# Kernel tuning notes

Hardware: AMD Instinct MI355X
Metric: run time of the kernel (lower is better)

The kernel has to match this reference:

```python
import jax, jax.numpy as jnp
import numpy as np

B, N, D_POINTS, D_MODEL = 2, 2048, 32, 512


def _gather(feat, idx):
    # feat: [B, N, C], idx: [B, N, K] -> [B, N, K, C]
    return jax.vmap(lambda f, i: f[i])(feat, idx)


def setup_inputs() -> dict:
    key = jax.random.key(0)
    ks = jax.random.split(key, 20)
    def lin(k, fan_in, fan_out):
        bound = 1.0 / np.sqrt(fan_in)
        return jax.random.uniform(k, (fan_in, fan_out), jnp.float32, -bound, bound)
    def bias(k, fan_in, fan_out):
        bound = 1.0 / np.sqrt(fan_in)
        return jax.random.uniform(k, (fan_out,), jnp.float32, -bound, bound)
    return {
        "xyz": jax.random.normal(ks[0], (B, N, 3), jnp.float32),
        "points": jax.random.normal(ks[1], (B, N, D_POINTS), jnp.float32),
        "fc1_w": lin(ks[2], D_POINTS, D_MODEL), "fc1_b": bias(ks[3], D_POINTS, D_MODEL),
        "fc2_w": lin(ks[4], D_MODEL, D_POINTS), "fc2_b": bias(ks[5], D_MODEL, D_POINTS),
        "delta_w1": lin(ks[6], 3, D_MODEL), "delta_b1": bias(ks[7], 3, D_MODEL),
        "delta_w2": lin(ks[8], D_MODEL, D_MODEL), "delta_b2": bias(ks[9], D_MODEL, D_MODEL),
        "gamma_w1": lin(ks[10], D_MODEL, D_MODEL), "gamma_b1": bias(ks[11], D_MODEL, D_MODEL),
        "gamma_w2": lin(ks[12], D_MODEL, D_MODEL), "gamma_b2": bias(ks[13], D_MODEL, D_MODEL),
        "wq": lin(ks[14], D_MODEL, D_MODEL),
        "wk": lin(ks[15], D_MODEL, D_MODEL),
        "wv": lin(ks[16], D_MODEL, D_MODEL),
        "knn_k": 16,
    }


def reference(xyz, points, fc1_w, fc1_b, fc2_w, fc2_b,
              delta_w1, delta_b1, delta_w2, delta_b2,
              gamma_w1, gamma_b1, gamma_w2, gamma_b2,
              wq, wk, wv, knn_k):
    # square_distance: [B, N, N]
    sq = jnp.sum(xyz * xyz, axis=-1)
    dists = sq[:, :, None] + sq[:, None, :] - 2.0 * jnp.einsum('bnc,bmc->bnm', xyz, xyz)
    # knn: k smallest distances (argsort[:, :, :k] equivalent)
    _, knn_idx = jax.lax.top_k(-dists, knn_k)           # [B, N, K]
    knn_xyz = _gather(xyz, knn_idx)                      # [B, N, K, 3]

    pre = points
    x = points @ fc1_w + fc1_b                           # [B, N, d_model]
    q = x @ wq                                           # [B, N, d_model]
    k = _gather(x @ wk, knn_idx)                         # [B, N, K, d_model]
    v = _gather(x @ wv, knn_idx)                         # [B, N, K, d_model]

    # positional encoding MLP on delta xyz
    delta = xyz[:, :, None, :] - knn_xyz                 # [B, N, K, 3]
    pos_enc = jax.nn.relu(delta @ delta_w1 + delta_b1) @ delta_w2 + delta_b2

    # gamma MLP on (q - k + pos_enc)
    a = q[:, :, None, :] - k + pos_enc
    a = jax.nn.relu(a @ gamma_w1 + gamma_b1) @ gamma_w2 + gamma_b2

    scale = jnp.asarray(np.sqrt(D_MODEL), a.dtype)
    attn = jax.nn.softmax(a / scale, axis=-2)            # softmax over neighbors, per channel

    res = jnp.sum(attn * (v + pos_enc), axis=2)          # einsum 'bmnf,bmnf->bmf'
    res = res @ fc2_w + fc2_b + pre                      # [B, N, d_points]
    return res, attn
```

## Files before the change

kernel.cpp:

```cpp
#include <hip/hip_runtime.h>
#include <hip/hip_bf16.h>
#include <math.h>

typedef __bf16 bf16_t;
typedef float f32x4 __attribute__((ext_vector_type(4)));
typedef bf16_t bf16x8 __attribute__((ext_vector_type(8)));

#define BM 128
#define BN 128
#define BKT 32
#define NT 16

#define GLD_LDS16(gp, lp) __builtin_amdgcn_global_load_lds( \
    (const __attribute__((address_space(1))) void*)(gp), \
    (__attribute__((address_space(3))) void*)(lp), 16, 0, 0)

struct TC7 { const float* src[7]; bf16_t* dst[7]; };
__global__ __launch_bounds__(256) void tcast7_kernel(TC7 tc) {
  int job = blockIdx.x >> 10;
  int idx = (blockIdx.x & 1023) * 256 + threadIdx.x;
  if (job < 4) {
    int n = idx >> 9, k = idx & 511;
    tc.dst[job][idx] = (bf16_t)tc.src[job][k * 512 + n];
  } else {
    tc.dst[job][idx] = (bf16_t)tc.src[job][idx];
  }
}

__global__ __launch_bounds__(256) void cc_kernel(const float* __restrict__ db2, const float* __restrict__ gw1,
                                                 const float* __restrict__ gb1, float* __restrict__ cc) {
  int n = blockIdx.x * 256 + threadIdx.x;
  float s = gb1[n];
  for (int d = 0; d < 512; ++d) s = fmaf(db2[d], gw1[d * 512 + n], s);
  cc[n] = s;
}

__global__ __launch_bounds__(256) void knn_kernel(const float* __restrict__ xyz, int* __restrict__ knn) {
  __shared__ float sx[2048], sy[2048], sz[2048], sq[2048];
  int tid = threadIdx.x;
  int lane = tid & 63, wave = tid >> 6;
  int gq = blockIdx.x * 4 + wave;
  int b  = gq >> 11;
  int base = b << 11;
  for (int p = tid; p < 2048; p += 256) {
    float x = xyz[(base + p) * 3 + 0];
    float y = xyz[(base + p) * 3 + 1];
    float z = xyz[(base + p) * 3 + 2];
    sx[p] = x; sy[p] = y; sz[p] = z;
    sq[p] = __fadd_rn(__fadd_rn(__fmul_rn(x, x), __fmul_rn(y, y)), __fmul_rn(z, z));
  }
  __syncthreads();
  int iq = gq & 2047;
  float qx = sx[iq], qy = sy[iq], qz = sz[iq], sqi = sq[iq];

  unsigned long long key[32];
  #pragma unroll
  for (int j = 0; j < 32; ++j) {
    int p = lane + j * 64;
    float d = __fmul_rn(sx[p], qx);
    d = fmaf(sy[p], qy, d);
    d = fmaf(sz[p], qz, d);
    float dist = __fsub_rn(__fadd_rn(sqi, sq[p]), __fmul_rn(2.0f, d));
    unsigned int bits = __float_as_uint(dist);
    unsigned int sk = bits ^ (unsigned int)(((int)bits >> 31) | 0x80000000);
    key[j] = ((unsigned long long)sk << 32) | (unsigned int)p;
  }

  int r = 0;
  #pragma unroll 1
  for (int s = 0; s < 16; ++s) {
    unsigned long long m = key[0];
    #pragma unroll
    for (int j = 1; j < 32; ++j) m = (key[j] < m) ? key[j] : m;
    #pragma unroll
    for (int off = 32; off > 0; off >>= 1) {
      unsigned long long o = (unsigned long long)__shfl_xor((long long)m, off);
      if (o < m) m = o;
    }
    if (lane == s) r = base + (int)(m & 0xFFFFFFFFu);
    #pragma unroll
    for (int j = 0; j < 32; ++j) key[j] = (key[j] == m) ? ~0ULL : key[j];
  }
  if (lane < 16) knn[gq * 16 + lane] = r;
}

__global__ __launch_bounds__(256) void xfeat_kernel(const float* __restrict__ points, const float* __restrict__ fc1_w,
                                                    const float* __restrict__ fc1_b, bf16_t* __restrict__ xb) {
  __shared__ float p[32];
  int m = blockIdx.x, tid = threadIdx.x;
  if (tid < 32) p[tid] = points[m * 32 + tid];
  __syncthreads();
  for (int c = tid; c < 512; c += 256) {
    float a = fc1_b[c];
    #pragma unroll
    for (int kk = 0; kk < 32; ++kk) a = fmaf(p[kk], fc1_w[kk * 512 + c], a);
    xb[m * 512 + c] = (bf16_t)a;
  }
}

__global__ __launch_bounds__(256) void final_kernel(const float* __restrict__ res_mid, const float* __restrict__ fc2_w,
                                                    const float* __restrict__ fc2_b, const float* __restrict__ points,
                                                    float* __restrict__ out) {
  int oid = blockIdx.x * 256 + threadIdx.x;
  int m = oid >> 5, c = oid & 31;
  float a = fc2_b[c];
  const float* rm = res_mid + m * 512;
  for (int kk = 0; kk < 512; ++kk) a = fmaf(rm[kk], fc2_w[kk * 32 + c], a);
  out[oid] = a + points[oid];
}

struct GP {
  const bf16_t* A; const bf16_t* Bt;
  bf16_t* Cb; const float* bias; int ldc;
  const float* xyz; const int* knn; const float* dw1; const float* db1;
  const float* cc; const bf16_t* qkg;
  const bf16_t* vb; const bf16_t* peb; float* attn; float* res_mid;
  const bf16_t* Aj[3]; bf16_t* Cbj[3];
};

template <int SRC, int EPI>
__global__ __launch_bounds__(256) void gemm_kernel(GP gp) {
  __shared__ bf16_t Alds[2 * BM * BKT];
  __shared__ bf16_t Blds[2 * BN * BKT];
  __shared__ float  wl[(SRC == 2) ? 4 * 512 : 8];
  int tid  = threadIdx.x;
  int lane = tid & 63, wave = tid >> 6;
  int wr = wave >> 1, wc = wave & 1;
  int lr = lane & 15, lg = lane >> 4;

  int gx = gridDim.x;
  int nwg = gx * gridDim.y;
  int orig = blockIdx.y * gx + blockIdx.x;
  int cpx = nwg >> 3;
  int swz = (orig & 7) * cpx + (orig >> 3);
  int bx = swz % gx;
  int by = swz / gx;
  int n0 = bx * BN;
  int m0 = ((EPI == 4) ? (by & 3) : by) * BM;
  const bf16_t* Aptr = (EPI == 4) ? gp.Aj[by >> 2] : gp.A;

  f32x4 acc[4][4];
  #pragma unroll
  for (int i = 0; i < 4; ++i)
    #pragma unroll
    for (int j = 0; j < 4; ++j) acc[i][j] = (f32x4){0.f, 0.f, 0.f, 0.f};

  int rS2 = tid >> 2;
  int sl  = tid & 3;
  int swb = (rS2 >> 1) & 3;
  int scS = ((sl ^ swb) << 3);

  float dx0, dy0, dz0, dx1, dy1, dz1;
  if (SRC == 2) {
    for (int c = tid; c < 512; c += 256) {
      wl[c]        = gp.dw1[c];
      wl[512 + c]  = gp.dw1[512 + c];
      wl[1024 + c] = gp.dw1[1024 + c];
      wl[1536 + c] = gp.db1[c];
    }
    int m_a = m0 + rS2, m_b = m0 + rS2 + 64;
    int ga = m_a >> 4, ja = gp.knn[m_a];
    int gb = m_b >> 4, jb = gp.knn[m_b];
    dx0 = gp.xyz[ga * 3 + 0] - gp.xyz[ja * 3 + 0];
    dy0 = gp.xyz[ga * 3 + 1] - gp.xyz[ja * 3 + 1];
    dz0 = gp.xyz[ga * 3 + 2] - gp.xyz[ja * 3 + 2];
    dx1 = gp.xyz[gb * 3 + 0] - gp.xyz[jb * 3 + 0];
    dy1 = gp.xyz[gb * 3 + 1] - gp.xyz[jb * 3 + 1];
    dz1 = gp.xyz[gb * 3 + 2] - gp.xyz[jb * 3 + 2];
    __syncthreads();
  }

  auto stageA = [&](int t, int buf) {
    int k0 = t * BKT;
    if (SRC == 0) {
      GLD_LDS16(Aptr + (size_t)(m0 + rS2) * 512 + k0 + scS,       Alds + buf * (BM * BKT) + tid * 8);
      GLD_LDS16(Aptr + (size_t)(m0 + 64 + rS2) * 512 + k0 + scS,  Alds + buf * (BM * BKT) + 2048 + tid * 8);
    } else {
      int cb = k0 + sl * 8;
      f32x4 w0a = *(const f32x4*)(&wl[cb]),        w0b = *(const f32x4*)(&wl[cb + 4]);
      f32x4 w1a = *(const f32x4*)(&wl[512 + cb]),  w1b = *(const f32x4*)(&wl[512 + cb + 4]);
      f32x4 w2a = *(const f32x4*)(&wl[1024 + cb]), w2b = *(const f32x4*)(&wl[1024 + cb + 4]);
      f32x4 bba = *(const f32x4*)(&wl[1536 + cb]), bbb = *(const f32x4*)(&wl[1536 + cb + 4]);
      bf16_t* Ab = Alds + buf * (BM * BKT);
      bf16x8 o;
      #pragma unroll
      for (int u = 0; u < 4; ++u) {
        float h = fmaf(dz0, w2a[u], fmaf(dy0, w1a[u], dx0 * w0a[u])) + bba[u];
        o[u] = (bf16_t)fmaxf(h, 0.0f);
      }
      #pragma unroll
      for (int u = 0; u < 4; ++u) {
        float h = fmaf(dz0, w2b[u], fmaf(dy0, w1b[u], dx0 * w0b[u])) + bbb[u];
        o[4 + u] = (bf16_t)fmaxf(h, 0.0f);
      }
      *(bf16x8*)(&Ab[rS2 * BKT + (scS ^ 0)]) = o;
      #pragma unroll
      for (int u = 0; u < 4; ++u) {
        float h = fmaf(dz1, w2a[u], fmaf(dy1, w1a[u], dx1 * w0a[u])) + bba[u];
        o[u] = (bf16_t)fmaxf(h, 0.0f);
      }
      #pragma unroll
      for (int u = 0; u < 4; ++u) {
        float h = fmaf(dz1, w2b[u], fmaf(dy1, w1b[u], dx1 * w0b[u])) + bbb[u];
        o[4 + u] = (bf16_t)fmaxf(h, 0.0f);
      }
      *(bf16x8*)(&Ab[(rS2 + 64) * BKT + (scS ^ 0)]) = o;
    }
  };
  auto stageB = [&](int t, int buf) {
    int k0 = t * BKT;
    GLD_LDS16(gp.Bt + (size_t)(n0 + rS2) * 512 + k0 + scS,       Blds + buf * (BN * BKT) + tid * 8);
    GLD_LDS16(gp.Bt + (size_t)(n0 + 64 + rS2) * 512 + k0 + scS,  Blds + buf * (BN * BKT) + 2048 + tid * 8);
  };
  auto mfmaPhase = [&](int cur) {
    const bf16_t* Ab = Alds + cur * (BM * BKT);
    const bf16_t* Bb = Blds + cur * (BN * BKT);
    bf16x8 af[4], bfr[4];
    #pragma unroll
    for (int mi = 0; mi < 4; ++mi) {
      int rr = wr * 64 + mi * 16 + lr;
      af[mi] = *(const bf16x8*)(&Ab[rr * BKT + ((lg ^ ((rr >> 1) & 3)) << 3)]);
    }
    #pragma unroll
    for (int nj = 0; nj < 4; ++nj) {
      int rr = wc * 64 + nj * 16 + lr;
      bfr[nj] = *(const bf16x8*)(&Bb[rr * BKT + ((lg ^ ((rr >> 1) & 3)) << 3)]);
    }
    #pragma unroll
    for (int mi = 0; mi < 4; ++mi)
      #pragma unroll
      for (int nj = 0; nj < 4; ++nj)
        acc[mi][nj] = __builtin_amdgcn_mfma_f32_16x16x32_bf16(af[mi], bfr[nj], acc[mi][nj], 0, 0, 0);
  };

  stageA(0, 0);
  stageB(0, 0);

  #pragma unroll 1
  for (int t = 0; t < NT; ++t) {
    int cur = t & 1;
    if (t + 1 < NT) {
      stageA(t + 1, cur ^ 1);
      stageB(t + 1, cur ^ 1);
      if (SRC == 0) asm volatile("s_waitcnt vmcnt(4)" ::: "memory");
      else          asm volatile("s_waitcnt vmcnt(2) lgkmcnt(0)" ::: "memory");
    } else {
      asm volatile("s_waitcnt vmcnt(0) lgkmcnt(0)" ::: "memory");
    }
    __builtin_amdgcn_s_barrier();
    mfmaPhase(cur);
    __builtin_amdgcn_s_barrier();
  }

  if (EPI == 4) {
    bf16_t* CbT = gp.Cbj[by >> 2];
    #pragma unroll
    for (int mi = 0; mi < 4; ++mi)
      #pragma unroll
      for (int nj = 0; nj < 4; ++nj) {
        int col = n0 + wc * 64 + nj * 16 + lr;
        #pragma unroll
        for (int r = 0; r < 4; ++r) {
          int row = m0 + wr * 64 + mi * 16 + lg * 4 + r;
          CbT[(size_t)col * 512 + row] = (bf16_t)acc[mi][nj][r];
        }
      }
  } else if (EPI == 6) {
    #pragma unroll
    for (int mi = 0; mi < 4; ++mi)
      #pragma unroll
      for (int nj = 0; nj < 4; ++nj) {
        int col = n0 + wc * 64 + nj * 16 + lr;
        int part = col >> 9, c = col & 511;
        #pragma unroll
        for (int r = 0; r < 4; ++r) {
          int row = m0 + wr * 64 + mi * 16 + lg * 4 + r;
          gp.Cb[((size_t)part * 4096 + row) * 512 + c] = (bf16_t)acc[mi][nj][r];
        }
      }
  } else if (EPI == 1) {
    #pragma unroll
    for (int mi = 0; mi < 4; ++mi)
      #pragma unroll
      for (int nj = 0; nj < 4; ++nj) {
        int col = n0 + wc * 64 + nj * 16 + lr;
        float bv = gp.bias[col];
        #pragma unroll
        for (int r = 0; r < 4; ++r) {
          int row = m0 + wr * 64 + mi * 16 + lg * 4 + r;
          gp.Cb[(size_t)row * 512 + col] = (bf16_t)(acc[mi][nj][r] + bv);
        }
      }
  } else if (EPI == 2) {
    #pragma unroll
    for (int mi = 0; mi < 4; ++mi) {
      int g = (m0 + wr * 64 + mi * 16) >> 4;
      #pragma unroll
      for (int nj = 0; nj < 4; ++nj) {
        int col = n0 + wc * 64 + nj * 16 + lr;
        float ccv = gp.cc[col];
        float qgv = (float)gp.qkg[((size_t)4096 + g) * 512 + col];
        #pragma unroll
        for (int r = 0; r < 4; ++r) {
          int row = m0 + wr * 64 + mi * 16 + lg * 4 + r;
          int j = gp.knn[row];
          float kgv = (float)gp.qkg[((size_t)2 * 4096 + j) * 512 + col];
          float hv = acc[mi][nj][r] + ccv + qgv - kgv;
          gp.Cb[(size_t)row * 512 + col] = (bf16_t)fmaxf(hv, 0.0f);
        }
      }
    }
  } else {
    const float scale = 22.62741699796952f;
    #pragma unroll
    for (int mi = 0; mi < 4; ++mi) {
      int g = (m0 + wr * 64 + mi * 16) >> 4;
      #pragma unroll
      for (int nj = 0; nj < 4; ++nj) {
        int col = n0 + wc * 64 + nj * 16 + lr;
        float sv[4];
        float mx = -INFINITY;
        #pragma unroll
        for (int r = 0; r < 4; ++r) {
          sv[r] = (acc[mi][nj][r] + gp.bias[col]) / scale;
          mx = fmaxf(mx, sv[r]);
        }
        mx = fmaxf(mx, __shfl_xor(mx, 16));
        mx = fmaxf(mx, __shfl_xor(mx, 32));
        float e[4], sum = 0.f;
        #pragma unroll
        for (int r = 0; r < 4; ++r) { e[r] = expf(sv[r] - mx); sum += e[r]; }
        sum += __shfl_xor(sum, 16);
        sum += __shfl_xor(sum, 32);
        float part = 0.f;
        #pragma unroll
        for (int r = 0; r < 4; ++r) {
          int row = g * 16 + lg * 4 + r;
          float at = e[r] / sum;
          int j = gp.knn[row];
          float vv  = (float)gp.vb[(size_t)j * 512 + col];
          float pev = (float)gp.peb[(size_t)row * 512 + col];
          part = fmaf(at, vv + pev, part);
          gp.attn[(size_t)row * 512 + col] = at;
        }
        part += __shfl_xor(part, 16);
        part += __shfl_xor(part, 32);
        if (lg == 0) gp.res_mid[(size_t)g * 512 + col] = part;
      }
    }
  }
}

extern "C" void kernel_launch(void* const* d_in, const int* in_sizes, int n_in,
                              void* d_out, int out_size, void* d_ws, size_t ws_size,
                              hipStream_t stream) {
  const float* xyz    = (const float*)d_in[0];
  const float* points = (const float*)d_in[1];
  const float* fc1_w  = (const float*)d_in[2];
  const float* fc1_b  = (const float*)d_in[3];
  const float* fc2_w  = (const float*)d_in[4];
  const float* fc2_b  = (const float*)d_in[5];
  const float* dw1    = (const float*)d_in[6];
  const float* db1    = (const float*)d_in[7];
  const float* dw2    = (const float*)d_in[8];
  const float* db2    = (const float*)d_in[9];
  const float* gw1    = (const float*)d_in[10];
  const float* gb1    = (const float*)d_in[11];
  const float* gw2    = (const float*)d_in[12];
  const float* gb2    = (const float*)d_in[13];
  const float* wq     = (const float*)d_in[14];
  const float* wk     = (const float*)d_in[15];
  const float* wv     = (const float*)d_in[16];

  float* out = (float*)d_out;
  float* attn = out + 131072;

  char* w = (char*)d_ws;
  bf16_t* wBig   = (bf16_t*)w; w += (size_t)1536 * 512 * 2;
  bf16_t* dw2T   = (bf16_t*)w; w += (size_t)512 * 512 * 2;
  bf16_t* gw1T   = (bf16_t*)w; w += (size_t)512 * 512 * 2;
  bf16_t* gw2T   = (bf16_t*)w; w += (size_t)512 * 512 * 2;
  bf16_t* dw2b   = (bf16_t*)w; w += (size_t)512 * 512 * 2;
  bf16_t* wqb    = (bf16_t*)w; w += (size_t)512 * 512 * 2;
  bf16_t* wkb    = (bf16_t*)w; w += (size_t)512 * 512 * 2;
  bf16_t* WpT    = (bf16_t*)w; w += (size_t)512 * 512 * 2;
  float*  cc     = (float*)w;  w += (size_t)512 * 4;
  int*    knn    = (int*)w;    w += (size_t)65536 * 4;
  bf16_t* xb     = (bf16_t*)w; w += (size_t)4096 * 512 * 2;
  bf16_t* vqkg   = (bf16_t*)w; w += (size_t)3 * 4096 * 512 * 2;
  bf16_t* peb    = (bf16_t*)w; w += (size_t)65536 * 512 * 2;
  bf16_t* h2     = (bf16_t*)w; w += (size_t)65536 * 512 * 2;
  float*  res_mid= (float*)w;  w += (size_t)4096 * 512 * 4;

  TC7 tc;
  tc.src[0] = wv;  tc.dst[0] = wBig;
  tc.src[1] = dw2; tc.dst[1] = dw2T;
  tc.src[2] = gw1; tc.dst[2] = gw1T;
  tc.src[3] = gw2; tc.dst[3] = gw2T;
  tc.src[4] = dw2; tc.dst[4] = dw2b;
  tc.src[5] = wq;  tc.dst[5] = wqb;
  tc.src[6] = wk;  tc.dst[6] = wkb;
  tcast7_kernel<<<7168, 256, 0, stream>>>(tc);

  knn_kernel<<<1024, 256, 0, stream>>>(xyz, knn);
  xfeat_kernel<<<4096, 256, 0, stream>>>(points, fc1_w, fc1_b, xb);
  cc_kernel<<<2, 256, 0, stream>>>(db2, gw1, gb1, cc);

  GP gwp{};
  gwp.Bt = gw1T;
  gwp.Aj[0] = dw2b; gwp.Cbj[0] = WpT;
  gwp.Aj[1] = wqb;  gwp.Cbj[1] = wBig + (size_t)512 * 512;
  gwp.Aj[2] = wkb;  gwp.Cbj[2] = wBig + (size_t)2 * 512 * 512;
  gemm_kernel<0, 4><<<dim3(4, 12), 256, 0, stream>>>(gwp);

  GP gq{};
  gq.A = xb; gq.Bt = wBig; gq.Cb = vqkg; gq.ldc = 1536;
  gemm_kernel<0, 6><<<dim3(12, 32), 256, 0, stream>>>(gq);

  GP gpe{};
  gpe.Bt = dw2T; gpe.Cb = peb; gpe.bias = db2;
  gpe.xyz = xyz; gpe.knn = knn; gpe.dw1 = dw1; gpe.db1 = db1;
  gemm_kernel<2, 1><<<dim3(4, 512), 256, 0, stream>>>(gpe);

  GP gg{};
  gg.Bt = WpT; gg.Cb = h2;
  gg.xyz = xyz; gg.knn = knn; gg.dw1 = dw1; gg.db1 = db1;
  gg.cc = cc; gg.qkg = vqkg;
  gemm_kernel<2, 2><<<dim3(4, 512), 256, 0, stream>>>(gg);

  GP gs{};
  gs.A = h2; gs.Bt = gw2T; gs.bias = gb2;
  gs.knn = knn; gs.vb = vqkg; gs.peb = peb; gs.attn = attn; gs.res_mid = res_mid;
  gemm_kernel<0, 3><<<dim3(4, 512), 256, 0, stream>>>(gs);

  final_kernel<<<512, 256, 0, stream>>>(res_mid, fc2_w, fc2_b, points, out);
}
```

Measured before the change: 436.7 us.

## Fuse pos-enc, gamma-hidden and softmax GEMMs into one register-resident kernel

Replaces the three per-neighbor GEMM launches (pos-enc, gamma layer 1, gamma layer 2 with softmax epilogue) with a single fused kernel. Each 64-row block keeps h2 and pos_enc in packed bf16 registers and re-shuffles them through a small LDS bounce buffer as MFMA A-operands. This removes the 64 MB peb and h2 intermediates and their global round trips. In exchange it carries heavy register pressure (64 u32 arrays), recomputes the h1 fragments twice, and uses a narrower N=64 M tile that may lower MFMA efficiency and occupancy.

```diff
diff --git a/kernel.cpp b/kernel.cpp
--- a/kernel.cpp
+++ b/kernel.cpp
@@ -5,15 +5,24 @@
 typedef __bf16 bf16_t;
 typedef float f32x4 __attribute__((ext_vector_type(4)));
 typedef bf16_t bf16x8 __attribute__((ext_vector_type(8)));
-
-#define BM 128
-#define BN 128
-#define BKT 32
-#define NT 16
+typedef unsigned int u32;
+typedef u32 u32x2 __attribute__((ext_vector_type(2)));
+typedef u32 u32x4 __attribute__((ext_vector_type(4)));
+typedef unsigned short u16x4 __attribute__((ext_vector_type(4)));
 
 #define GLD_LDS16(gp, lp) __builtin_amdgcn_global_load_lds( \
     (const __attribute__((address_space(1))) void*)(gp), \
     (__attribute__((address_space(3))) void*)(lp), 16, 0, 0)
+
+static __device__ __forceinline__ unsigned short f2b(float f) {
+  union { bf16_t b; unsigned short s; } u; u.b = (bf16_t)f; return u.s;
+}
+static __device__ __forceinline__ float b2f(unsigned short s) {
+  union { unsigned int i; float f; } u; u.i = ((unsigned)s) << 16; return u.f;
+}
+static __device__ __forceinline__ u32 packbf(float a, float b) {
+  return (u32)f2b(a) | ((u32)f2b(b) << 16);
+}
 
 struct TC7 { const float* src[7]; bf16_t* dst[7]; };
 __global__ __launch_bounds__(256) void tcast7_kernel(TC7 tc) {
@@ -110,19 +119,14 @@
 }
 
 struct GP {
-  const bf16_t* A; const bf16_t* Bt;
-  bf16_t* Cb; const float* bias; int ldc;
-  const float* xyz; const int* knn; const float* dw1; const float* db1;
-  const float* cc; const bf16_t* qkg;
-  const bf16_t* vb; const bf16_t* peb; float* attn; float* res_mid;
+  const bf16_t* A; const bf16_t* Bt; bf16_t* Cb; int ldc;
   const bf16_t* Aj[3]; bf16_t* Cbj[3];
 };
 
-template <int SRC, int EPI>
+template <int EPI>
 __global__ __launch_bounds__(256) void gemm_kernel(GP gp) {
-  __shared__ bf16_t Alds[2 * BM * BKT];
-  __shared__ bf16_t Blds[2 * BN * BKT];
-  __shared__ float  wl[(SRC == 2) ? 4 * 512 : 8];
+  __shared__ bf16_t Alds[2 * 128 * 32];
+  __shared__ bf16_t Blds[2 * 128 * 32];
   int tid  = threadIdx.x;
   int lane = tid & 63, wave = tid >> 6;
   int wr = wave >> 1, wc = wave & 1;
@@ -135,8 +139,8 @@
   int swz = (orig & 7) * cpx + (orig >> 3);
   int bx = swz % gx;
   int by = swz / gx;
-  int n0 = bx * BN;
-  int m0 = ((EPI == 4) ? (by & 3) : by) * BM;
+  int n0 = bx * 128;
+  int m0 = ((EPI == 4) ? (by & 3) : by) * 128;
   const bf16_t* Aptr = (EPI == 4) ? gp.Aj[by >> 2] : gp.A;
 
   f32x4 acc[4][4];
@@ -146,109 +150,52 @@
     for (int j = 0; j < 4; ++j) acc[i][j] = (f32x4){0.f, 0.f, 0.f, 0.f};
 
   int rS2 = tid >> 2;
-  int sl  = tid & 3;
   int swb = (rS2 >> 1) & 3;
-  int scS = ((sl ^ swb) << 3);
-
-  float dx0, dy0, dz0, dx1, dy1, dz1;
-  if (SRC == 2) {
-    for (int c = tid; c < 512; c += 256) {
-      wl[c]        = gp.dw1[c];
-      wl[512 + c]  = gp.dw1[512 + c];
-      wl[1024 + c] = gp.dw1[1024 + c];
-      wl[1536 + c] = gp.db1[c];
-    }
-    int m_a = m0 + rS2, m_b = m0 + rS2 + 64;
-    int ga = m_a >> 4, ja = gp.knn[m_a];
-    int gb = m_b >> 4, jb = gp.knn[m_b];
-    dx0 = gp.xyz[ga * 3 + 0] - gp.xyz[ja * 3 + 0];
-    dy0 = gp.xyz[ga * 3 + 1] - gp.xyz[ja * 3 + 1];
-    dz0 = gp.xyz[ga * 3 + 2] - gp.xyz[ja * 3 + 2];
-    dx1 = gp.xyz[gb * 3 + 0] - gp.xyz[jb * 3 + 0];
-    dy1 = gp.xyz[gb * 3 + 1] - gp.xyz[jb * 3 + 1];
-    dz1 = gp.xyz[gb * 3 + 2] - gp.xyz[jb * 3 + 2];
-    __syncthreads();
-  }
+  int scS = (((tid & 3) ^ swb) << 3);
 
   auto stageA = [&](int t, int buf) {
-    int k0 = t * BKT;
-    if (SRC == 0) {
-      GLD_LDS16(Aptr + (size_t)(m0 + rS2) * 512 + k0 + scS,       Alds + buf * (BM * BKT) + tid * 8);
-      GLD_LDS16(Aptr + (size_t)(m0 + 64 + rS2) * 512 + k0 + scS,  Alds + buf * (BM * BKT) + 2048 + tid * 8);
-    } else {
-      int cb = k0 + sl * 8;
-      f32x4 w0a = *(const f32x4*)(&wl[cb]),        w0b = *(const f32x4*)(&wl[cb + 4]);
-      f32x4 w1a = *(const f32x4*)(&wl[512 + cb]),  w1b = *(const f32x4*)(&wl[512 + cb + 4]);
-      f32x4 w2a = *(const f32x4*)(&wl[1024 + cb]), w2b = *(const f32x4*)(&wl[1024 + cb + 4]);
-      f32x4 bba = *(const f32x4*)(&wl[1536 + cb]), bbb = *(const f32x4*)(&wl[1536 + cb + 4]);
-      bf16_t* Ab = Alds + buf * (BM * BKT);
-      bf16x8 o;
-      #pragma unroll
-      for (int u = 0; u < 4; ++u) {
-        float h = fmaf(dz0, w2a[u], fmaf(dy0, w1a[u], dx0 * w0a[u])) + bba[u];
-        o[u] = (bf16_t)fmaxf(h, 0.0f);
-      }
-      #pragma unroll
-      for (int u = 0; u < 4; ++u) {
-        float h = fmaf(dz0, w2b[u], fmaf(dy0, w1b[u], dx0 * w0b[u])) + bbb[u];
-        o[4 + u] = (bf16_t)fmaxf(h, 0.0f);
-      }
-      *(bf16x8*)(&Ab[rS2 * BKT + (scS ^ 0)]) = o;
-      #pragma unroll
-      for (int u = 0; u < 4; ++u) {
-        float h = fmaf(dz1, w2a[u], fmaf(dy1, w1a[u], dx1 * w0a[u])) + bba[u];
-        o[u] = (bf16_t)fmaxf(h, 0.0f);
-      }
-      #pragma unroll
-      for (int u = 0; u < 4; ++u) {
-        float h = fmaf(dz1, w2b[u], fmaf(dy1, w1b[u], dx1 * w0b[u])) + bbb[u];
-        o[4 + u] = (bf16_t)fmaxf(h, 0.0f);
-      }
-      *(bf16x8*)(&Ab[(rS2 + 64) * BKT + (scS ^ 0)]) = o;
-    }
+    int k0 = t * 32;
+    GLD_LDS16(Aptr + (size_t)(m0 + rS2) * 512 + k0 + scS,       Alds + buf * 4096 + tid * 8);
+    GLD_LDS16(Aptr + (size_t)(m0 + 64 + rS2) * 512 + k0 + scS,  Alds + buf * 4096 + 2048 + tid * 8);
   };
   auto stageB = [&](int t, int buf) {
-    int k0 = t * BKT;
-    GLD_LDS16(gp.Bt + (size_t)(n0 + rS2) * 512 + k0 + scS,       Blds + buf * (BN * BKT) + tid * 8);
-    GLD_LDS16(gp.Bt + (size_t)(n0 + 64 + rS2) * 512 + k0 + scS,  Blds + buf * (BN * BKT) + 2048 + tid * 8);
+    int k0 = t * 32;
+    GLD_LDS16(gp.Bt + (size_t)(n0 + rS2) * 512 + k0 + scS,       Blds + buf * 4096 + tid * 8);
+    GLD_LDS16(gp.Bt + (size_t)(n0 + 64 + rS2) * 512 + k0 + scS,  Blds + buf * 4096 + 2048 + tid * 8);
   };
-  auto mfmaPhase = [&](int cur) {
-    const bf16_t* Ab = Alds + cur * (BM * BKT);
-    const bf16_t* Bb = Blds + cur * (BN * BKT);
+
+  stageA(0, 0);
+  stageB(0, 0);
+
+  #pragma unroll 1
+  for (int t = 0; t < 16; ++t) {
+    int cur = t & 1;
+    if (t + 1 < 16) {
+      stageA(t + 1, cur ^ 1);
+      stageB(t + 1, cur ^ 1);
+      asm volatile("s_waitcnt vmcnt(4)" ::: "memory");
+    } else {
+      asm volatile("s_waitcnt vmcnt(0)" ::: "memory");
+    }
+    __builtin_amdgcn_s_barrier();
+    const bf16_t* Ab = Alds + cur * 4096;
+    const bf16_t* Bb = Blds + cur * 4096;
     bf16x8 af[4], bfr[4];
     #pragma unroll
     for (int mi = 0; mi < 4; ++mi) {
       int rr = wr * 64 + mi * 16 + lr;
-      af[mi] = *(const bf16x8*)(&Ab[rr * BKT + ((lg ^ ((rr >> 1) & 3)) << 3)]);
+      af[mi] = *(const bf16x8*)(&Ab[rr * 32 + ((lg ^ ((rr >> 1) & 3)) << 3)]);
     }
     #pragma unroll
     for (int nj = 0; nj < 4; ++nj) {
       int rr = wc * 64 + nj * 16 + lr;
-      bfr[nj] = *(const bf16x8*)(&Bb[rr * BKT + ((lg ^ ((rr >> 1) & 3)) << 3)]);
+      bfr[nj] = *(const bf16x8*)(&Bb[rr * 32 + ((lg ^ ((rr >> 1) & 3)) << 3)]);
     }
     #pragma unroll
     for (int mi = 0; mi < 4; ++mi)
       #pragma unroll
       for (int nj = 0; nj < 4; ++nj)
         acc[mi][nj] = __builtin_amdgcn_mfma_f32_16x16x32_bf16(af[mi], bfr[nj], acc[mi][nj], 0, 0, 0);
-  };
-
-  stageA(0, 0);
-  stageB(0, 0);
-
-  #pragma unroll 1
-  for (int t = 0; t < NT; ++t) {
-    int cur = t & 1;
-    if (t + 1 < NT) {
-      stageA(t + 1, cur ^ 1);
-      stageB(t + 1, cur ^ 1);
-      if (SRC == 0) asm volatile("s_waitcnt vmcnt(4)" ::: "memory");
-      else          asm volatile("s_waitcnt vmcnt(2) lgkmcnt(0)" ::: "memory");
-    } else {
-      asm volatile("s_waitcnt vmcnt(0) lgkmcnt(0)" ::: "memory");
-    }
-    __builtin_amdgcn_s_barrier();
-    mfmaPhase(cur);
     __builtin_amdgcn_s_barrier();
   }
 
@@ -265,7 +212,7 @@
           CbT[(size_t)col * 512 + row] = (bf16_t)acc[mi][nj][r];
         }
       }
-  } else if (EPI == 6) {
+  } else {
     #pragma unroll
     for (int mi = 0; mi < 4; ++mi)
       #pragma unroll
@@ -278,75 +225,214 @@
           gp.Cb[((size_t)part * 4096 + row) * 512 + c] = (bf16_t)acc[mi][nj][r];
         }
       }
-  } else if (EPI == 1) {
-    #pragma unroll
-    for (int mi = 0; mi < 4; ++mi)
-      #pragma unroll
-      for (int nj = 0; nj < 4; ++nj) {
-        int col = n0 + wc * 64 + nj * 16 + lr;
-        float bv = gp.bias[col];
-        #pragma unroll
-        for (int r = 0; r < 4; ++r) {
-          int row = m0 + wr * 64 + mi * 16 + lg * 4 + r;
-          gp.Cb[(size_t)row * 512 + col] = (bf16_t)(acc[mi][nj][r] + bv);
-        }
+  }
+}
+
+struct FP {
+  const float* xyz; const int* knn;
+  const float* dw1; const float* db1; const float* db2; const float* cc; const float* gb2;
+  const bf16_t* WpT; const bf16_t* dw2T; const bf16_t* gw2T;
+  const bf16_t* vqkg;
+  float* attn; float* res_mid;
+};
+
+__global__ __launch_bounds__(256, 2) void fused_kernel(FP fp) {
+  __shared__ float  wl[3584];
+  __shared__ bf16_t Bst[2 * 128 * 32];
+  __shared__ u32    bounce[4 * 256];
+
+  int tid = threadIdx.x, lane = tid & 63, w = tid >> 6;
+  int lr = lane & 15, lg = lane >> 4;
+
+  int nwg = gridDim.x, orig = blockIdx.x, cpx = nwg >> 3;
+  int bid = (orig & 7) * cpx + (orig >> 3);
+  int m0 = bid * 64;
+  int g  = (m0 >> 4) + w;
+  int myrow = m0 + w * 16 + lr;
+  int j_lane = fp.knn[myrow];
+  float dx = fp.xyz[g * 3 + 0] - fp.xyz[j_lane * 3 + 0];
+  float dy = fp.xyz[g * 3 + 1] - fp.xyz[j_lane * 3 + 1];
+  float dz = fp.xyz[g * 3 + 2] - fp.xyz[j_lane * 3 + 2];
+
+  for (int c = tid; c < 1536; c += 256) wl[c] = fp.dw1[c];
+  for (int c = tid; c < 512; c += 256) {
+    wl[1536 + c] = fp.db1[c];
+    wl[2048 + c] = fp.cc[c];
+    wl[2560 + c] = fp.db2[c];
+    wl[3072 + c] = fp.gb2[c];
+  }
+  __syncthreads();
+
+  auto h1frag = [&](int st) -> bf16x8 {
+    int c = st * 32 + lg * 8;
+    f32x4 w0a = *(const f32x4*)&wl[c],        w0b = *(const f32x4*)&wl[c + 4];
+    f32x4 w1a = *(const f32x4*)&wl[512 + c],  w1b = *(const f32x4*)&wl[512 + c + 4];
+    f32x4 w2a = *(const f32x4*)&wl[1024 + c], w2b = *(const f32x4*)&wl[1024 + c + 4];
+    f32x4 ba  = *(const f32x4*)&wl[1536 + c], bb = *(const f32x4*)&wl[1536 + c + 4];
+    bf16x8 o;
+    #pragma unroll
+    for (int u = 0; u < 4; ++u) {
+      float h = fmaf(dz, w2a[u], fmaf(dy, w1a[u], dx * w0a[u])) + ba[u];
+      o[u] = (bf16_t)fmaxf(h, 0.0f);
+    }
+    #pragma unroll
+    for (int u = 0; u < 4; ++u) {
+      float h = fmaf(dz, w2b[u], fmaf(dy, w1b[u], dx * w0b[u])) + bb[u];
+      o[4 + u] = (bf16_t)fmaxf(h, 0.0f);
+    }
+    return o;
+  };
+
+  int rS2 = tid >> 2;
+  int scS = (((tid & 3) ^ ((rS2 >> 1) & 3)) << 3);
+  auto stage = [&](const bf16_t* Bt, int base, int st, int buf) {
+    GLD_LDS16(Bt + (size_t)(base + rS2) * 512 + st * 32 + scS,      Bst + buf * 4096 + tid * 8);
+    GLD_LDS16(Bt + (size_t)(base + 64 + rS2) * 512 + st * 32 + scS, Bst + buf * 4096 + 2048 + tid * 8);
+  };
+  auto bfrag = [&](int buf, int tt) -> bf16x8 {
+    int rr = tt * 16 + lr;
+    return *(const bf16x8*)(&Bst[buf * 4096 + rr * 32 + ((lg ^ ((rr >> 1) & 3)) << 3)]);
+  };
+
+  u32 h2pk[32][2];
+  u32 pepk[32][2];
+
+  #pragma unroll
+  for (int mc = 0; mc < 4; ++mc) {
+    f32x4 acc1[8];
+    #pragma unroll
+    for (int i = 0; i < 8; ++i) acc1[i] = (f32x4){0.f, 0.f, 0.f, 0.f};
+    stage(fp.WpT, mc * 128, 0, 0);
+    #pragma unroll 1
+    for (int st = 0; st < 16; ++st) {
+      if (st < 15) {
+        stage(fp.WpT, mc * 128, st + 1, (st & 1) ^ 1);
+        asm volatile("s_waitcnt vmcnt(2)" ::: "memory");
+      } else {
+        asm volatile("s_waitcnt vmcnt(0)" ::: "memory");
       }
-  } else if (EPI == 2) {
-    #pragma unroll
-    for (int mi = 0; mi < 4; ++mi) {
-      int g = (m0 + wr * 64 + mi * 16) >> 4;
-      #pragma unroll
-      for (int nj = 0; nj < 4; ++nj) {
-        int col = n0 + wc * 64 + nj * 16 + lr;
-        float ccv = gp.cc[col];
-        float qgv = (float)gp.qkg[((size_t)4096 + g) * 512 + col];
-        #pragma unroll
-        for (int r = 0; r < 4; ++r) {
-          int row = m0 + wr * 64 + mi * 16 + lg * 4 + r;
-          int j = gp.knn[row];
-          float kgv = (float)gp.qkg[((size_t)2 * 4096 + j) * 512 + col];
-          float hv = acc[mi][nj][r] + ccv + qgv - kgv;
-          gp.Cb[(size_t)row * 512 + col] = (bf16_t)fmaxf(hv, 0.0f);
-        }
+      __builtin_amdgcn_s_barrier();
+      bf16x8 bh = h1frag(st);
+      #pragma unroll
+      for (int tt = 0; tt < 8; ++tt)
+        acc1[tt] = __builtin_amdgcn_mfma_f32_16x16x32_bf16(bfrag(st & 1, tt), bh, acc1[tt], 0, 0, 0);
+      __builtin_amdgcn_s_barrier();
+    }
+    #pragma unroll
+    for (int tt = 0; tt < 8; ++tt) {
+      int c0 = mc * 128 + tt * 16 + lg * 4;
+      u16x4 kg4 = *(const u16x4*)((const unsigned short*)fp.vqkg + ((size_t)2 * 4096 + j_lane) * 512 + c0);
+      u16x4 qg4 = *(const u16x4*)((const unsigned short*)fp.vqkg + ((size_t)4096 + g) * 512 + c0);
+      f32x4 cc4 = *(const f32x4*)&wl[2048 + c0];
+      float hv[4];
+      #pragma unroll
+      for (int r = 0; r < 4; ++r)
+        hv[r] = fmaxf(acc1[tt][r] + cc4[r] + b2f(qg4[r]) - b2f(kg4[r]), 0.0f);
+      h2pk[mc * 8 + tt][0] = packbf(hv[0], hv[1]);
+      h2pk[mc * 8 + tt][1] = packbf(hv[2], hv[3]);
+    }
+  }
+
+  #pragma unroll
+  for (int nc = 0; nc < 4; ++nc) {
+    f32x4 acc2[8];
+    #pragma unroll
+    for (int i = 0; i < 8; ++i) acc2[i] = (f32x4){0.f, 0.f, 0.f, 0.f};
+    stage(fp.dw2T, nc * 128, 0, 0);
+    #pragma unroll 1
+    for (int st = 0; st < 16; ++st) {
+      if (st < 15) {
+        stage(fp.dw2T, nc * 128, st + 1, (st & 1) ^ 1);
+        asm volatile("s_waitcnt vmcnt(2)" ::: "memory");
+      } else {
+        asm volatile("s_waitcnt vmcnt(0)" ::: "memory");
       }
-    }
-  } else {
-    const float scale = 22.62741699796952f;
-    #pragma unroll
-    for (int mi = 0; mi < 4; ++mi) {
-      int g = (m0 + wr * 64 + mi * 16) >> 4;
-      #pragma unroll
-      for (int nj = 0; nj < 4; ++nj) {
-        int col = n0 + wc * 64 + nj * 16 + lr;
-        float sv[4];
-        float mx = -INFINITY;
-        #pragma unroll
-        for (int r = 0; r < 4; ++r) {
-          sv[r] = (acc[mi][nj][r] + gp.bias[col]) / scale;
-          mx = fmaxf(mx, sv[r]);
-        }
-        mx = fmaxf(mx, __shfl_xor(mx, 16));
-        mx = fmaxf(mx, __shfl_xor(mx, 32));
-        float e[4], sum = 0.f;
-        #pragma unroll
-        for (int r = 0; r < 4; ++r) { e[r] = expf(sv[r] - mx); sum += e[r]; }
-        sum += __shfl_xor(sum, 16);
-        sum += __shfl_xor(sum, 32);
-        float part = 0.f;
-        #pragma unroll
-        for (int r = 0; r < 4; ++r) {
-          int row = g * 16 + lg * 4 + r;
-          float at = e[r] / sum;
-          int j = gp.knn[row];
-          float vv  = (float)gp.vb[(size_t)j * 512 + col];
-          float pev = (float)gp.peb[(size_t)row * 512 + col];
-          part = fmaf(at, vv + pev, part);
-          gp.attn[(size_t)row * 512 + col] = at;
-        }
-        part += __shfl_xor(part, 16);
-        part += __shfl_xor(part, 32);
-        if (lg == 0) gp.res_mid[(size_t)g * 512 + col] = part;
+      __builtin_amdgcn_s_barrier();
+      bf16x8 ah = h1frag(st);
+      #pragma unroll
+      for (int tt = 0; tt < 8; ++tt)
+        acc2[tt] = __builtin_amdgcn_mfma_f32_16x16x32_bf16(ah, bfrag(st & 1, tt), acc2[tt], 0, 0, 0);
+      __builtin_amdgcn_s_barrier();
+    }
+    #pragma unroll
+    for (int tt = 0; tt < 8; ++tt) {
+      int col = nc * 128 + tt * 16 + lr;
+      float d2 = wl[2560 + col];
+      pepk[nc * 8 + tt][0] = packbf(acc2[tt][0] + d2, acc2[tt][1] + d2);
+      pepk[nc * 8 + tt][1] = packbf(acc2[tt][2] + d2, acc2[tt][3] + d2);
+    }
+  }
+
+  u32* bw = &bounce[w * 256];
+  int wrOff = lane * 4;
+  int rdA = (lr + ((lg & 1) << 5)) * 4 + (lg >> 1) * 2;
+  int rdB = rdA + 64;
+  int jr[4];
+  #pragma unroll
+  for (int r = 0; r < 4; ++r) jr[r] = __shfl(j_lane, lg * 4 + r);
+
+  const float scale = 22.62741699796952f;
+
+  #pragma unroll
+  for (int nc = 0; nc < 4; ++nc) {
+    f32x4 acc3[8];
+    #pragma unroll
+    for (int i = 0; i < 8; ++i) acc3[i] = (f32x4){0.f, 0.f, 0.f, 0.f};
+    stage(fp.gw2T, nc * 128, 0, 0);
+
+#define P3STEP(ST) { \
+    if ((ST) < 15) { stage(fp.gw2T, nc * 128, (ST) + 1, ((ST) & 1) ^ 1); \
+                     asm volatile("s_waitcnt vmcnt(2)" ::: "memory"); } \
+    else           { asm volatile("s_waitcnt vmcnt(0)" ::: "memory"); } \
+    __builtin_amdgcn_s_barrier(); \
+    *(u32x4*)(bw + wrOff) = (u32x4){h2pk[2*(ST)][0], h2pk[2*(ST)][1], h2pk[2*(ST)+1][0], h2pk[2*(ST)+1][1]}; \
+    asm volatile("s_waitcnt lgkmcnt(0)" ::: "memory"); \
+    union { bf16x8 v; u32x2 h[2]; } afu; \
+    afu.h[0] = *(const u32x2*)(bw + rdA); \
+    afu.h[1] = *(const u32x2*)(bw + rdB); \
+    _Pragma("unroll") \
+    for (int tt = 0; tt < 8; ++tt) \
+      acc3[tt] = __builtin_amdgcn_mfma_f32_16x16x32_bf16(afu.v, bfrag((ST) & 1, tt), acc3[tt], 0, 0, 0); \
+    __builtin_amdgcn_s_barrier(); }
+
+    P3STEP(0)  P3STEP(1)  P3STEP(2)  P3STEP(3)
+    P3STEP(4)  P3STEP(5)  P3STEP(6)  P3STEP(7)
+    P3STEP(8)  P3STEP(9)  P3STEP(10) P3STEP(11)
+    P3STEP(12) P3STEP(13) P3STEP(14) P3STEP(15)
+#undef P3STEP
+
+    #pragma unroll
+    for (int tt = 0; tt < 8; ++tt) {
+      int col = nc * 128 + tt * 16 + lr;
+      float gb2v = wl[3072 + col];
+      float sv[4];
+      float mx = -INFINITY;
+      #pragma unroll
+      for (int r = 0; r < 4; ++r) {
+        sv[r] = (acc3[tt][r] + gb2v) / scale;
+        mx = fmaxf(mx, sv[r]);
       }
+      mx = fmaxf(mx, __shfl_xor(mx, 16));
+      mx = fmaxf(mx, __shfl_xor(mx, 32));
+      float e[4], sum = 0.f;
+      #pragma unroll
+      for (int r = 0; r < 4; ++r) { e[r] = expf(sv[r] - mx); sum += e[r]; }
+      sum += __shfl_xor(sum, 16);
+      sum += __shfl_xor(sum, 32);
+      float part = 0.f;
+      #pragma unroll
+      for (int r = 0; r < 4; ++r) {
+        int row = g * 16 + lg * 4 + r;
+        float at = e[r] / sum;
+        float vv = (float)fp.vqkg[(size_t)jr[r] * 512 + col];
+        u32 pw = pepk[nc * 8 + tt][r >> 1];
+        float pev = b2f((unsigned short)(pw >> (16 * (r & 1))));
+        part = fmaf(at, vv + pev, part);
+        fp.attn[(size_t)row * 512 + col] = at;
+      }
+      part += __shfl_xor(part, 16);
+      part += __shfl_xor(part, 32);
+      if (lg == 0) fp.res_mid[(size_t)g * 512 + col] = part;
     }
   }
 }
@@ -388,8 +474,6 @@
   int*    knn    = (int*)w;    w += (size_t)65536 * 4;
   bf16_t* xb     = (bf16_t*)w; w += (size_t)4096 * 512 * 2;
   bf16_t* vqkg   = (bf16_t*)w; w += (size_t)3 * 4096 * 512 * 2;
-  bf16_t* peb    = (bf16_t*)w; w += (size_t)65536 * 512 * 2;
-  bf16_t* h2     = (bf16_t*)w; w += (size_t)65536 * 512 * 2;
   float*  res_mid= (float*)w;  w += (size_t)4096 * 512 * 4;
 
   TC7 tc;
@@ -411,27 +495,19 @@
   gwp.Aj[0] = dw2b; gwp.Cbj[0] = WpT;
   gwp.Aj[1] = wqb;  gwp.Cbj[1] = wBig + (size_t)512 * 512;
   gwp.Aj[2] = wkb;  gwp.Cbj[2] = wBig + (size_t)2 * 512 * 512;
-  gemm_kernel<0, 4><<<dim3(4, 12), 256, 0, stream>>>(gwp);
+  gemm_kernel<4><<<dim3(4, 12), 256, 0, stream>>>(gwp);
 
   GP gq{};
   gq.A = xb; gq.Bt = wBig; gq.Cb = vqkg; gq.ldc = 1536;
-  gemm_kernel<0, 6><<<dim3(12, 32), 256, 0, stream>>>(gq);
-
-  GP gpe{};
-  gpe.Bt = dw2T; gpe.Cb = peb; gpe.bias = db2;
-  gpe.xyz = xyz; gpe.knn = knn; gpe.dw1 = dw1; gpe.db1 = db1;
-  gemm_kernel<2, 1><<<dim3(4, 512), 256, 0, stream>>>(gpe);
-
-  GP gg{};
-  gg.Bt = WpT; gg.Cb = h2;
-  gg.xyz = xyz; gg.knn = knn; gg.dw1 = dw1; gg.db1 = db1;
-  gg.cc = cc; gg.qkg = vqkg;
-  gemm_kernel<2, 2><<<dim3(4, 512), 256, 0, stream>>>(gg);
-
-  GP gs{};
-  gs.A = h2; gs.Bt = gw2T; gs.bias = gb2;
-  gs.knn = knn; gs.vb = vqkg; gs.peb = peb; gs.attn = attn; gs.res_mid = res_mid;
-  gemm_kernel<0, 3><<<dim3(4, 512), 256, 0, stream>>>(gs);
+  gemm_kernel<6><<<dim3(12, 32), 256, 0, stream>>>(gq);
+
+  FP fp{};
+  fp.xyz = xyz; fp.knn = knn;
+  fp.dw1 = dw1; fp.db1 = db1; fp.db2 = db2; fp.cc = cc; fp.gb2 = gb2;
+  fp.WpT = WpT; fp.dw2T = dw2T; fp.gw2T = gw2T;
+  fp.vqkg = vqkg;
+  fp.attn = attn; fp.res_mid = res_mid;
+  fused_kernel<<<1024, 256, 0, stream>>>(fp);
 
   final_kernel<<<512, 256, 0, stream>>>(res_mid, fc2_w, fc2_b, points, out);
 }
```

New measurement: 695.7 us. 1.59x slower.
